# Optimization experiments

Hardware: AMD Instinct MI355X
Metric: run time of the kernel (lower is better)

The kernel has to match this reference:

```python
import jax, jax.numpy as jnp
import numpy as np
from math import sqrt

N_HEADS = 4
IN_FEATURES = 64
KQ = 64
HEAD_V = IN_FEATURES // N_HEADS  # 16


def setup_inputs() -> dict:
    key = jax.random.key(0)
    ks = jax.random.split(key, 7)
    s = 0.05
    x = jax.random.normal(ks[0], (8192, IN_FEATURES), dtype=jnp.float32)
    # Per-head Linear weights stacked on a leading head axis.
    # torch Linear: y = x @ W.T + b; we store W already transposed: [H, F, E]
    Wq = jax.random.normal(ks[1], (N_HEADS, IN_FEATURES, KQ), dtype=jnp.float32) * s
    bq = jax.random.normal(ks[2], (N_HEADS, KQ), dtype=jnp.float32) * s
    Wk = jax.random.normal(ks[3], (N_HEADS, IN_FEATURES, KQ), dtype=jnp.float32) * s
    bk = jax.random.normal(ks[4], (N_HEADS, KQ), dtype=jnp.float32) * s
    Wv = jax.random.normal(ks[5], (N_HEADS, IN_FEATURES, HEAD_V), dtype=jnp.float32) * s
    bv = jax.random.normal(ks[6], (N_HEADS, HEAD_V), dtype=jnp.float32) * s
    return {"x": x, "Wq": Wq, "bq": bq, "Wk": Wk, "bk": bk, "Wv": Wv, "bv": bv}


def reference(x, Wq, bq, Wk, bk, Wv, bv):
    N, F = x.shape
    scale = 1.0 / sqrt(F)  # original divides by sqrt(in_features), NOT sqrt(kq)
    # Batched-head projections: [H, N, E]
    Q = jnp.einsum('nf,hfe->hne', x, Wq) + bq[:, None, :]
    K = jnp.einsum('nf,hfe->hne', x, Wk) + bk[:, None, :]
    V = jnp.einsum('nf,hfd->hnd', x, Wv) + bv[:, None, :]
    logits = jnp.einsum('hne,hme->hnm', Q, K) * scale  # [H, N, N]
    attn = jax.nn.softmax(logits, axis=-1)
    out_heads = jnp.einsum('hnm,hmd->hnd', attn, V)    # [H, N, HEAD_V]
    # Head i writes columns [i*HEAD_V:(i+1)*HEAD_V] of the output.
    out = jnp.transpose(out_heads, (1, 0, 2)).reshape(N, F)
    return out
```

## Files before the change

kernel.cpp:

```cpp
#include <hip/hip_runtime.h>

typedef __attribute__((ext_vector_type(4))) float f32x4;
typedef __attribute__((ext_vector_type(8))) short bf16x8;
typedef __attribute__((ext_vector_type(4))) short bf16x4;
typedef long fp8x8;

#define NH 4

static __device__ __forceinline__ unsigned short f2bf(float f){
  unsigned u = __float_as_uint(f);
  u += 0x7FFFu + ((u >> 16) & 1u);
  return (unsigned short)(u >> 16);
}

static __device__ __forceinline__ unsigned pack2bf(float a, float b){
  return __builtin_amdgcn_perm(__float_as_uint(b) + 0x8000u,
                               __float_as_uint(a) + 0x8000u, 0x07060302u);
}

static __device__ __forceinline__ unsigned pack2bf_t(float a, float b){
  return __builtin_amdgcn_perm(__float_as_uint(b), __float_as_uint(a), 0x07060302u);
}

static __device__ __forceinline__ int pack_fp8x4(float a, float b, float c, float d){
  int w = __builtin_amdgcn_cvt_pk_fp8_f32(a, b, 0, false);
  w     = __builtin_amdgcn_cvt_pk_fp8_f32(c, d, w, true);
  return w;
}

__global__ __launch_bounds__(256) void wprep_kernel(
    const float* __restrict__ Wq, const float* __restrict__ bq,
    const float* __restrict__ Wk, const float* __restrict__ bk,
    const float* __restrict__ Wv,
    unsigned short* __restrict__ WF, float* __restrict__ bias_s, int n)
{
  __shared__ unsigned short wqT[64*72];
  __shared__ unsigned short wkT[64*72];
  __shared__ unsigned short wvT[16*72];

  const int t = threadIdx.x;
  const int h = blockIdx.x;
  const float S1 = 0.4246609001f;
  const int f = t >> 2, eg = t & 3;

  {
    const float4* g = (const float4*)(Wq + h*4096 + f*64 + eg*16);
    #pragma unroll
    for (int p = 0; p < 4; ++p){
      float4 d = g[p];
      int e0 = eg*16 + p*4;
      wqT[(e0+0)*72 + f] = f2bf(d.x * S1);
      wqT[(e0+1)*72 + f] = f2bf(d.y * S1);
      wqT[(e0+2)*72 + f] = f2bf(d.z * S1);
      wqT[(e0+3)*72 + f] = f2bf(d.w * S1);
    }
  }
  {
    const float4* g = (const float4*)(Wk + h*4096 + f*64 + eg*16);
    #pragma unroll
    for (int p = 0; p < 4; ++p){
      float4 d = g[p];
      int e0 = eg*16 + p*4;
      wkT[(e0+0)*72 + f] = f2bf(d.x * S1);
      wkT[(e0+1)*72 + f] = f2bf(d.y * S1);
      wkT[(e0+2)*72 + f] = f2bf(d.z * S1);
      wkT[(e0+3)*72 + f] = f2bf(d.w * S1);
    }
  }
  {
    float4 d = *(const float4*)(Wv + h*1024 + f*16 + eg*4);
    int d0 = eg*4;
    wvT[(d0+0)*72 + f] = f2bf(d.x);
    wvT[(d0+1)*72 + f] = f2bf(d.y);
    wvT[(d0+2)*72 + f] = f2bf(d.z);
    wvT[(d0+3)*72 + f] = f2bf(d.w);
  }
  if (t < 64)       bias_s[h*128 + t] = bq[h*64 + t] * S1;
  else if (t < 128) bias_s[h*128 + t] = bk[h*64 + (t-64)] * S1;
  __syncthreads();

  const int lane = t & 63, w = t >> 6;
  const int quad = lane >> 4, l16 = lane & 15;
  for (int s = w; s < 18; s += 4){
    const unsigned short* src;
    if (s < 8){      int et = s>>1,     ks = s&1;     src = wqT + (et*16+l16)*72 + ks*32 + quad*8; }
    else if (s < 16){int ft = (s-8)>>1, ks = (s-8)&1; src = wkT + (ft*16+l16)*72 + ks*32 + quad*8; }
    else {           int ks = s-16;                   src = wvT + l16*72 + ks*32 + quad*8; }
    uint4 v = *(const uint4*)src;
    *(uint4*)(WF + ((size_t)(h*18 + s)*64 + lane)*8) = v;
  }
}

__global__ __launch_bounds__(256) void proj_kernel(
    const float* __restrict__ x, const float* __restrict__ bv,
    const unsigned short* __restrict__ WF, const float* __restrict__ bias_s,
    unsigned char* __restrict__ Qfr, unsigned char* __restrict__ Kt,
    unsigned short* __restrict__ Vt, int n)
{
  __shared__ unsigned short xf[8*64*8];
  __shared__ float bql[64], bkl[64], bvl[16];

  const int t  = threadIdx.x;
  const int h  = blockIdx.y;
  const int r0 = blockIdx.x * 64;

  {
    const int r = t >> 2, cg4 = t & 3;
    const float4* g = (const float4*)(x + (size_t)(r0 + r)*64 + cg4*16);
    float4 a = g[0], b = g[1], c = g[2], d = g[3];
    unsigned u0 = pack2bf(a.x,a.y), u1 = pack2bf(a.z,a.w);
    unsigned u2 = pack2bf(b.x,b.y), u3 = pack2bf(b.z,b.w);
    unsigned u4 = pack2bf(c.x,c.y), u5 = pack2bf(c.z,c.w);
    unsigned u6 = pack2bf(d.x,d.y), u7 = pack2bf(d.z,d.w);
    const int it = r >> 4, l16r = r & 15, ks = cg4 >> 1, q0 = (cg4 & 1)*2;
    uint4* dst0 = (uint4*)(xf + ((it*2+ks)*64 + q0*16     + l16r)*8);
    uint4* dst1 = (uint4*)(xf + ((it*2+ks)*64 + (q0+1)*16 + l16r)*8);
    *dst0 = make_uint4(u0,u1,u2,u3);
    *dst1 = make_uint4(u4,u5,u6,u7);
  }
  if (t < 64)        bql[t]     = bias_s[h*128 + t];
  else if (t < 128)  bkl[t-64]  = bias_s[h*128 + t];
  else if (t < 144)  bvl[t-128] = bv[h*16 + (t-128)];
  __syncthreads();

  const int lane = t & 63, w = t >> 6;
  const int quad = lane >> 4, l16 = lane & 15;

  bf16x8 xa[8];
  #pragma unroll
  for (int i = 0; i < 8; ++i)
    xa[i] = *(const bf16x8*)(xf + (i*64 + lane)*8);

  const unsigned short* WFh = WF + (size_t)h*18*64*8;
  bf16x8 wq0 = *(const bf16x8*)(WFh + ((size_t)(     w*2 + 0)*64 + lane)*8);
  bf16x8 wq1 = *(const bf16x8*)(WFh + ((size_t)(     w*2 + 1)*64 + lane)*8);
  bf16x8 wk0 = *(const bf16x8*)(WFh + ((size_t)(8  + w*2 + 0)*64 + lane)*8);
  bf16x8 wk1 = *(const bf16x8*)(WFh + ((size_t)(8  + w*2 + 1)*64 + lane)*8);
  bf16x8 wv0 = *(const bf16x8*)(WFh + ((size_t)16*64 + lane)*8);
  bf16x8 wv1 = *(const bf16x8*)(WFh + ((size_t)17*64 + lane)*8);

  const f32x4 z = {0.f,0.f,0.f,0.f};
  f32x4 accQ[4] = {z,z,z,z};
  f32x4 accK[4] = {z,z,z,z};
  f32x4 accV = z;

  #pragma unroll
  for (int it = 0; it < 4; ++it){
    accQ[it] = __builtin_amdgcn_mfma_f32_16x16x32_bf16(wq0, xa[it*2+0], accQ[it], 0,0,0);
    accQ[it] = __builtin_amdgcn_mfma_f32_16x16x32_bf16(wq1, xa[it*2+1], accQ[it], 0,0,0);
  }
  #pragma unroll
  for (int tt = 0; tt < 4; ++tt){
    accK[tt] = __builtin_amdgcn_mfma_f32_16x16x32_bf16(wk0, xa[tt*2+0], accK[tt], 0,0,0);
    accK[tt] = __builtin_amdgcn_mfma_f32_16x16x32_bf16(wk1, xa[tt*2+1], accK[tt], 0,0,0);
  }
  accV = __builtin_amdgcn_mfma_f32_16x16x32_bf16(xa[w*2+0], wv0, accV, 0,0,0);
  accV = __builtin_amdgcn_mfma_f32_16x16x32_bf16(xa[w*2+1], wv1, accV, 0,0,0);

  {
    const int e0 = w*16 + quad*4;
    const float b0 = bql[e0], b1 = bql[e0+1], b2 = bql[e0+2], b3 = bql[e0+3];
    const int qk = (e0 & 31) >> 3, hf = e0 >> 5, boff = (quad & 1) * 4;
    #pragma unroll
    for (int it = 0; it < 4; ++it){
      unsigned o = pack_fp8x4(accQ[it][0]+b0, accQ[it][1]+b1,
                              accQ[it][2]+b2, accQ[it][3]+b3);
      const int T = (r0 >> 4) + it;
      *(unsigned*)(Qfr + (size_t)h*((size_t)n<<6) + (size_t)T*1024
                       + (qk*16 + l16)*16 + hf*8 + boff) = o;
    }
  }
  {
    const int f0 = w*16 + quad*4;
    const float bk0 = bkl[f0], bk1 = bkl[f0+1], bk2 = bkl[f0+2], bk3 = bkl[f0+3];
    const int qk = (f0 & 31) >> 3, hf = f0 >> 5, boff = (quad & 1) * 4;
    #pragma unroll
    for (int tt = 0; tt < 4; ++tt){
      unsigned o = pack_fp8x4(accK[tt][0]+bk0, accK[tt][1]+bk1,
                              accK[tt][2]+bk2, accK[tt][3]+bk3);
      const int T = (r0 >> 4) + tt;
      *(unsigned*)(Kt + (size_t)h*((size_t)n<<6) + (size_t)T*1024
                      + (qk*16 + l16)*16 + hf*8 + boff) = o;
    }
  }
  {
    float bvv = bvl[l16];
    unsigned v01 = pack2bf(accV[0]+bvv, accV[1]+bvv);
    unsigned v23 = pack2bf(accV[2]+bvv, accV[3]+bvv);
    const int T = (r0 >> 4) + w;
    *(uint2*)(Vt + (size_t)h*((size_t)n<<4)
                 + ((size_t)(T>>1)*64 + lane)*8 + (T&1)*4) = make_uint2(v01, v23);
  }
}

__global__ __launch_bounds__(512, 4) void attn_kernel(
    const unsigned char* __restrict__ Qfr, const unsigned char* __restrict__ Kt,
    const unsigned short* __restrict__ Vt, float* __restrict__ out, int n)
{
  __shared__ float part[7][64][33];

  const int tid  = threadIdx.x;
  const int lane = tid & 63;
  const int jq   = tid >> 6;

  #pragma unroll 1
  for (int i = 0; i < jq; ++i) __builtin_amdgcn_s_sleep(3);

  const int bid  = blockIdx.x;
  const int h    = bid & 3;
  const int iblk = bid >> 2;
  const int l16  = lane & 15, quad = lane >> 4;
  const int i0   = iblk*64;
  const int ntq  = (n >> 3) >> 4;
  const int nch  = ntq >> 1;
  const int tile0 = jq * ntq;

  const unsigned char* qfh = Qfr + (size_t)h*((size_t)n<<6);
  longlong2 q0 = *(const longlong2*)(qfh + (size_t)((i0>>4)    )*1024 + lane*16);
  longlong2 q1 = *(const longlong2*)(qfh + (size_t)((i0>>4) + 1)*1024 + lane*16);
  longlong2 q2 = *(const longlong2*)(qfh + (size_t)((i0>>4) + 2)*1024 + lane*16);
  longlong2 q3 = *(const longlong2*)(qfh + (size_t)((i0>>4) + 3)*1024 + lane*16);
  const fp8x8 qf00 = (fp8x8)q0.x, qf01 = (fp8x8)q0.y;
  const fp8x8 qf10 = (fp8x8)q1.x, qf11 = (fp8x8)q1.y;
  const fp8x8 qf20 = (fp8x8)q2.x, qf21 = (fp8x8)q2.y;
  const fp8x8 qf30 = (fp8x8)q3.x, qf31 = (fp8x8)q3.y;

  const longlong2* ktl = (const longlong2*)(Kt + (size_t)h*((size_t)n<<6)) + (size_t)tile0*64 + lane;
  const uint4*     vtu = (const uint4*)(Vt + (size_t)h*((size_t)n<<4)) + (size_t)(tile0>>1)*64 + lane;

  const f32x4 z = {0.f,0.f,0.f,0.f};
  f32x4 o0 = z, o1 = z, o2 = z, o3 = z;
  f32x4 la0 = z, la1 = z, la2 = z, la3 = z;
  const bf16x8 vones = {(short)0x3F80, (short)0x3F80, (short)0x3F80, (short)0x3F80,
                        (short)0x3F80, (short)0x3F80, (short)0x3F80, (short)0x3F80};

  longlong2 ka0 = ktl[0],   ka1 = ktl[64];
  uint4     va  = vtu[0];
  longlong2 kb0 = ktl[128], kb1 = ktl[192];
  uint4     vb  = vtu[64];

#define ITILE(QA, QB, OO, LL)                                                 \
  {                                                                           \
    f32x4 s = __builtin_amdgcn_mfma_f32_16x16x32_fp8_fp8(a0, QA, z, 0,0,0);   \
    s = __builtin_amdgcn_mfma_f32_16x16x32_fp8_fp8(a1, QB, s, 0,0,0);         \
    f32x4 u = __builtin_amdgcn_mfma_f32_16x16x32_fp8_fp8(b0, QA, z, 0,0,0);   \
    u = __builtin_amdgcn_mfma_f32_16x16x32_fp8_fp8(b1, QB, u, 0,0,0);         \
    float e0 = __builtin_amdgcn_exp2f(s[0]);                                  \
    float e1 = __builtin_amdgcn_exp2f(s[1]);                                  \
    float e2 = __builtin_amdgcn_exp2f(s[2]);                                  \
    float e3 = __builtin_amdgcn_exp2f(s[3]);                                  \
    float f0 = __builtin_amdgcn_exp2f(u[0]);                                  \
    float f1 = __builtin_amdgcn_exp2f(u[1]);                                  \
    float f2 = __builtin_amdgcn_exp2f(u[2]);                                  \
    float f3 = __builtin_amdgcn_exp2f(u[3]);                                  \
    union { uint4 uu; bf16x8 v; } pq;                                         \
    pq.uu = make_uint4(pack2bf_t(e0,e1), pack2bf_t(e2,e3),                    \
                       pack2bf_t(f0,f1), pack2bf_t(f2,f3));                   \
    OO = __builtin_amdgcn_mfma_f32_16x16x32_bf16(pq.v, vfv,   OO, 0,0,0);     \
    LL = __builtin_amdgcn_mfma_f32_16x16x32_bf16(pq.v, vones, LL, 0,0,0);     \
  }

#define ATTN_CHUNK(KA, KB, VV)                                                \
  {                                                                           \
    const fp8x8 a0 = (fp8x8)KA.x, a1 = (fp8x8)KA.y;                           \
    const fp8x8 b0 = (fp8x8)KB.x, b1 = (fp8x8)KB.y;                           \
    union { uint4 uu; bf16x8 v; } vfu; vfu.uu = VV;                           \
    const bf16x8 vfv = vfu.v;                                                 \
    ITILE(qf00, qf01, o0, la0)                                                \
    ITILE(qf10, qf11, o1, la1)                                                \
    ITILE(qf20, qf21, o2, la2)                                                \
    ITILE(qf30, qf31, o3, la3)                                                \
  }

  for (int c = 0; c < nch - 2; c += 2){
    ATTN_CHUNK(ka0, ka1, va)
    ka0 = ktl[256]; ka1 = ktl[320]; va = vtu[128];
    ATTN_CHUNK(kb0, kb1, vb)
    kb0 = ktl[384]; kb1 = ktl[448]; vb = vtu[192];
    ktl += 256; vtu += 128;
    #pragma unroll
    for (int g = 0; g < 12; ++g){
      __builtin_amdgcn_sched_group_barrier(0x008, 2, 0);
      __builtin_amdgcn_sched_group_barrier(0x002, 8, 0);
    }
  }
  ATTN_CHUNK(ka0, ka1, va)
  ATTN_CHUNK(kb0, kb1, vb)
#undef ATTN_CHUNK
#undef ITILE

  if (jq > 0){
    float* p = &part[jq-1][lane][0];
    p[ 0]=o0[0];  p[ 1]=o0[1];  p[ 2]=o0[2];  p[ 3]=o0[3];
    p[ 4]=o1[0];  p[ 5]=o1[1];  p[ 6]=o1[2];  p[ 7]=o1[3];
    p[ 8]=o2[0];  p[ 9]=o2[1];  p[10]=o2[2];  p[11]=o2[3];
    p[12]=o3[0];  p[13]=o3[1];  p[14]=o3[2];  p[15]=o3[3];
    p[16]=la0[0]; p[17]=la0[1]; p[18]=la0[2]; p[19]=la0[3];
    p[20]=la1[0]; p[21]=la1[1]; p[22]=la1[2]; p[23]=la1[3];
    p[24]=la2[0]; p[25]=la2[1]; p[26]=la2[2]; p[27]=la2[3];
    p[28]=la3[0]; p[29]=la3[1]; p[30]=la3[2]; p[31]=la3[3];
  }
  __syncthreads();

  if (jq == 0){
    #pragma unroll
    for (int q = 0; q < 7; ++q){
      const float* r = &part[q][lane][0];
      o0[0] +=r[0];  o0[1] +=r[1];  o0[2] +=r[2];  o0[3] +=r[3];
      o1[0] +=r[4];  o1[1] +=r[5];  o1[2] +=r[6];  o1[3] +=r[7];
      o2[0] +=r[8];  o2[1] +=r[9];  o2[2] +=r[10]; o2[3] +=r[11];
      o3[0] +=r[12]; o3[1] +=r[13]; o3[2] +=r[14]; o3[3] +=r[15];
      la0[0]+=r[16]; la0[1]+=r[17]; la0[2]+=r[18]; la0[3]+=r[19];
      la1[0]+=r[20]; la1[1]+=r[21]; la1[2]+=r[22]; la1[3]+=r[23];
      la2[0]+=r[24]; la2[1]+=r[25]; la2[2]+=r[26]; la2[3]+=r[27];
      la3[0]+=r[28]; la3[1]+=r[29]; la3[2]+=r[30]; la3[3]+=r[31];
    }
    #pragma unroll
    for (int reg = 0; reg < 4; ++reg){
      int i = quad*4 + reg;
      out[(size_t)(i0 +      i)*64 + h*16 + l16] = o0[reg] / la0[reg];
      out[(size_t)(i0 + 16 + i)*64 + h*16 + l16] = o1[reg] / la1[reg];
      out[(size_t)(i0 + 32 + i)*64 + h*16 + l16] = o2[reg] / la2[reg];
      out[(size_t)(i0 + 48 + i)*64 + h*16 + l16] = o3[reg] / la3[reg];
    }
  }
}

extern "C" void kernel_launch(void* const* d_in, const int* in_sizes, int n_in,
                              void* d_out, int out_size, void* d_ws, size_t ws_size,
                              hipStream_t stream) {
  const float* x  = (const float*)d_in[0];
  const float* Wq = (const float*)d_in[1];
  const float* bq = (const float*)d_in[2];
  const float* Wk = (const float*)d_in[3];
  const float* bk = (const float*)d_in[4];
  const float* Wv = (const float*)d_in[5];
  const float* bv = (const float*)d_in[6];
  float* out = (float*)d_out;

  const int n = in_sizes[0] / 64;

  unsigned char* Qfr  = (unsigned char*)d_ws;
  unsigned char* Kt   = Qfr + (size_t)NH*n*64;
  unsigned short* Vt  = (unsigned short*)(Kt + (size_t)NH*n*64);
  unsigned short* WF  = Vt + (size_t)NH*n*16;
  float* bias_s       = (float*)(WF + (size_t)NH*18*64*8);

  wprep_kernel<<<NH, 256, 0, stream>>>(Wq, bq, Wk, bk, Wv, WF, bias_s, n);
  proj_kernel<<<dim3(n/64, NH), 256, 0, stream>>>(x, bv, WF, bias_s, Qfr, Kt, Vt, n);
  attn_kernel<<<dim3((n/64)*NH), 512, 0, stream>>>(Qfr, Kt, Vt, out, n);
}
```

Before: 118.5 us.

## Switch attention to 32x32 MFMA tiles with fused row-sum column

Rewrites the attention inner loop to use 32x32x64 scaled FP8 MFMAs for QK^T and 32x32x16 bf16 MFMAs for PV. Q/K/V are stored in a new 32-row-group layout to match. The softmax denominator now comes from a ones-column placed in the V operand's spare columns, removing the separate row-sum MFMA. permlane32_swap rearranges the probabilities between the two 32-lane halves. The aim is fewer MFMA issues and more work per instruction, at the cost of wasting half the PV tile width and adding select and lane-swap overhead.

```diff
diff --git a/kernel.cpp b/kernel.cpp
--- a/kernel.cpp
+++ b/kernel.cpp
@@ -1,8 +1,10 @@
 #include <hip/hip_runtime.h>
 
 typedef __attribute__((ext_vector_type(4))) float f32x4;
+typedef __attribute__((ext_vector_type(16))) float f32x16;
 typedef __attribute__((ext_vector_type(8))) short bf16x8;
-typedef __attribute__((ext_vector_type(4))) short bf16x4;
+typedef __attribute__((ext_vector_type(8))) int int32x8;
+typedef __attribute__((ext_vector_type(2))) int int32x2;
 typedef long fp8x8;
 
 #define NH 4
@@ -26,6 +28,10 @@
   int w = __builtin_amdgcn_cvt_pk_fp8_f32(a, b, 0, false);
   w     = __builtin_amdgcn_cvt_pk_fp8_f32(c, d, w, true);
   return w;
+}
+
+static __device__ __forceinline__ uint4 selv(bool c, uint4 a, uint4 b){
+  return make_uint4(c?a.x:b.x, c?a.y:b.y, c?a.z:b.z, c?a.w:b.w);
 }
 
 __global__ __launch_bounds__(256) void wprep_kernel(
@@ -47,8 +53,7 @@
     const float4* g = (const float4*)(Wq + h*4096 + f*64 + eg*16);
     #pragma unroll
     for (int p = 0; p < 4; ++p){
-      float4 d = g[p];
-      int e0 = eg*16 + p*4;
+      float4 d = g[p]; int e0 = eg*16 + p*4;
       wqT[(e0+0)*72 + f] = f2bf(d.x * S1);
       wqT[(e0+1)*72 + f] = f2bf(d.y * S1);
       wqT[(e0+2)*72 + f] = f2bf(d.z * S1);
@@ -59,8 +64,7 @@
     const float4* g = (const float4*)(Wk + h*4096 + f*64 + eg*16);
     #pragma unroll
     for (int p = 0; p < 4; ++p){
-      float4 d = g[p];
-      int e0 = eg*16 + p*4;
+      float4 d = g[p]; int e0 = eg*16 + p*4;
       wkT[(e0+0)*72 + f] = f2bf(d.x * S1);
       wkT[(e0+1)*72 + f] = f2bf(d.y * S1);
       wkT[(e0+2)*72 + f] = f2bf(d.z * S1);
@@ -157,39 +161,45 @@
   accV = __builtin_amdgcn_mfma_f32_16x16x32_bf16(xa[w*2+0], wv0, accV, 0,0,0);
   accV = __builtin_amdgcn_mfma_f32_16x16x32_bf16(xa[w*2+1], wv1, accV, 0,0,0);
 
+  const int kh    = w >> 1;
+  const int ebyte = (w & 1)*16 + quad*4;
+
   {
     const int e0 = w*16 + quad*4;
     const float b0 = bql[e0], b1 = bql[e0+1], b2 = bql[e0+2], b3 = bql[e0+3];
-    const int qk = (e0 & 31) >> 3, hf = e0 >> 5, boff = (quad & 1) * 4;
     #pragma unroll
     for (int it = 0; it < 4; ++it){
       unsigned o = pack_fp8x4(accQ[it][0]+b0, accQ[it][1]+b1,
                               accQ[it][2]+b2, accQ[it][3]+b3);
-      const int T = (r0 >> 4) + it;
-      *(unsigned*)(Qfr + (size_t)h*((size_t)n<<6) + (size_t)T*1024
-                       + (qk*16 + l16)*16 + hf*8 + boff) = o;
+      const int qg = (r0 >> 5) + (it >> 1);
+      const int lq = (it & 1)*16 + l16 + 32*kh;
+      *(unsigned*)(Qfr + (size_t)h*((size_t)n<<6)
+                       + ((size_t)(qg*64 + lq))*32 + ebyte) = o;
     }
   }
   {
     const int f0 = w*16 + quad*4;
     const float bk0 = bkl[f0], bk1 = bkl[f0+1], bk2 = bkl[f0+2], bk3 = bkl[f0+3];
-    const int qk = (f0 & 31) >> 3, hf = f0 >> 5, boff = (quad & 1) * 4;
     #pragma unroll
     for (int tt = 0; tt < 4; ++tt){
       unsigned o = pack_fp8x4(accK[tt][0]+bk0, accK[tt][1]+bk1,
                               accK[tt][2]+bk2, accK[tt][3]+bk3);
-      const int T = (r0 >> 4) + tt;
-      *(unsigned*)(Kt + (size_t)h*((size_t)n<<6) + (size_t)T*1024
-                      + (qk*16 + l16)*16 + hf*8 + boff) = o;
-    }
-  }
-  {
+      const int kg = (r0 >> 5) + (tt >> 1);
+      const int lk = (tt & 1)*16 + l16 + 32*kh;
+      *(unsigned*)(Kt + (size_t)h*((size_t)n<<6)
+                      + ((size_t)(kg*64 + lk))*32 + ebyte) = o;
+    }
+  }
+  {
+    const int T = (r0 >> 4) + w;
     float bvv = bvl[l16];
-    unsigned v01 = pack2bf(accV[0]+bvv, accV[1]+bvv);
-    unsigned v23 = pack2bf(accV[2]+bvv, accV[3]+bvv);
-    const int T = (r0 >> 4) + w;
-    *(uint2*)(Vt + (size_t)h*((size_t)n<<4)
-                 + ((size_t)(T>>1)*64 + lane)*8 + (T&1)*4) = make_uint2(v01, v23);
+    #pragma unroll
+    for (int reg = 0; reg < 4; ++reg){
+      const int key = quad*4 + reg;
+      Vt[(size_t)h*((size_t)n<<4)
+         + ((size_t)(T*32 + l16 + 16*(key>>3)))*8 + (key & 7)]
+        = f2bf(accV[reg] + bvv);
+    }
   }
 }
 
@@ -209,96 +219,100 @@
   const int bid  = blockIdx.x;
   const int h    = bid & 3;
   const int iblk = bid >> 2;
-  const int l16  = lane & 15, quad = lane >> 4;
   const int i0   = iblk*64;
-  const int ntq  = (n >> 3) >> 4;
-  const int nch  = ntq >> 1;
-  const int tile0 = jq * ntq;
-
-  const unsigned char* qfh = Qfr + (size_t)h*((size_t)n<<6);
-  longlong2 q0 = *(const longlong2*)(qfh + (size_t)((i0>>4)    )*1024 + lane*16);
-  longlong2 q1 = *(const longlong2*)(qfh + (size_t)((i0>>4) + 1)*1024 + lane*16);
-  longlong2 q2 = *(const longlong2*)(qfh + (size_t)((i0>>4) + 2)*1024 + lane*16);
-  longlong2 q3 = *(const longlong2*)(qfh + (size_t)((i0>>4) + 3)*1024 + lane*16);
-  const fp8x8 qf00 = (fp8x8)q0.x, qf01 = (fp8x8)q0.y;
-  const fp8x8 qf10 = (fp8x8)q1.x, qf11 = (fp8x8)q1.y;
-  const fp8x8 qf20 = (fp8x8)q2.x, qf21 = (fp8x8)q2.y;
-  const fp8x8 qf30 = (fp8x8)q3.x, qf31 = (fp8x8)q3.y;
-
-  const longlong2* ktl = (const longlong2*)(Kt + (size_t)h*((size_t)n<<6)) + (size_t)tile0*64 + lane;
-  const uint4*     vtu = (const uint4*)(Vt + (size_t)h*((size_t)n<<4)) + (size_t)(tile0>>1)*64 + lane;
-
-  const f32x4 z = {0.f,0.f,0.f,0.f};
-  f32x4 o0 = z, o1 = z, o2 = z, o3 = z;
-  f32x4 la0 = z, la1 = z, la2 = z, la3 = z;
-  const bf16x8 vones = {(short)0x3F80, (short)0x3F80, (short)0x3F80, (short)0x3F80,
-                        (short)0x3F80, (short)0x3F80, (short)0x3F80, (short)0x3F80};
-
-  longlong2 ka0 = ktl[0],   ka1 = ktl[64];
-  uint4     va  = vtu[0];
-  longlong2 kb0 = ktl[128], kb1 = ktl[192];
-  uint4     vb  = vtu[64];
-
-#define ITILE(QA, QB, OO, LL)                                                 \
+  const int c31  = lane & 31, hl = lane >> 5;
+  const int nch  = n >> 8;
+
+  const int32x8* qp = (const int32x8*)(Qfr + (size_t)h*((size_t)n<<6));
+  const int qg0 = i0 >> 5;
+  const int32x8 qA = qp[(size_t)qg0*64 + lane];
+  const int32x8 qB = qp[(size_t)(qg0+1)*64 + lane];
+
+  const int32x8* kp = (const int32x8*)(Kt + (size_t)h*((size_t)n<<6))
+                      + (size_t)(jq*32)*64 + lane;
+  const int vlane = (lane & 15) + ((lane & 32) >> 1);
+  const uint4* vp = (const uint4*)(Vt + (size_t)h*((size_t)n<<4))
+                    + (size_t)(jq*64)*32 + vlane;
+
+  const bool  vload = (c31 < 16);
+  const unsigned one2 = 0x3F803F80u;
+  const uint4 vsel = (c31 == 16) ? make_uint4(one2,one2,one2,one2)
+                                 : make_uint4(0,0,0,0);
+
+  const f32x16 z16 = {0,0,0,0,0,0,0,0,0,0,0,0,0,0,0,0};
+  f32x16 acc0 = z16, acc1 = z16;
+
+  int32x8 ka = kp[0], kb = kp[64];
+
+#define PVSTEP(S, ACC, VF0, VF1)                                              \
   {                                                                           \
-    f32x4 s = __builtin_amdgcn_mfma_f32_16x16x32_fp8_fp8(a0, QA, z, 0,0,0);   \
-    s = __builtin_amdgcn_mfma_f32_16x16x32_fp8_fp8(a1, QB, s, 0,0,0);         \
-    f32x4 u = __builtin_amdgcn_mfma_f32_16x16x32_fp8_fp8(b0, QA, z, 0,0,0);   \
-    u = __builtin_amdgcn_mfma_f32_16x16x32_fp8_fp8(b1, QB, u, 0,0,0);         \
-    float e0 = __builtin_amdgcn_exp2f(s[0]);                                  \
-    float e1 = __builtin_amdgcn_exp2f(s[1]);                                  \
-    float e2 = __builtin_amdgcn_exp2f(s[2]);                                  \
-    float e3 = __builtin_amdgcn_exp2f(s[3]);                                  \
-    float f0 = __builtin_amdgcn_exp2f(u[0]);                                  \
-    float f1 = __builtin_amdgcn_exp2f(u[1]);                                  \
-    float f2 = __builtin_amdgcn_exp2f(u[2]);                                  \
-    float f3 = __builtin_amdgcn_exp2f(u[3]);                                  \
-    union { uint4 uu; bf16x8 v; } pq;                                         \
-    pq.uu = make_uint4(pack2bf_t(e0,e1), pack2bf_t(e2,e3),                    \
-                       pack2bf_t(f0,f1), pack2bf_t(f2,f3));                   \
-    OO = __builtin_amdgcn_mfma_f32_16x16x32_bf16(pq.v, vfv,   OO, 0,0,0);     \
-    LL = __builtin_amdgcn_mfma_f32_16x16x32_bf16(pq.v, vones, LL, 0,0,0);     \
-  }
-
-#define ATTN_CHUNK(KA, KB, VV)                                                \
+    float p0  = __builtin_amdgcn_exp2f(S[0]);                                 \
+    float p1  = __builtin_amdgcn_exp2f(S[1]);                                 \
+    float p2  = __builtin_amdgcn_exp2f(S[2]);                                 \
+    float p3  = __builtin_amdgcn_exp2f(S[3]);                                 \
+    float p4  = __builtin_amdgcn_exp2f(S[4]);                                 \
+    float p5  = __builtin_amdgcn_exp2f(S[5]);                                 \
+    float p6  = __builtin_amdgcn_exp2f(S[6]);                                 \
+    float p7  = __builtin_amdgcn_exp2f(S[7]);                                 \
+    float p8  = __builtin_amdgcn_exp2f(S[8]);                                 \
+    float p9  = __builtin_amdgcn_exp2f(S[9]);                                 \
+    float p10 = __builtin_amdgcn_exp2f(S[10]);                                \
+    float p11 = __builtin_amdgcn_exp2f(S[11]);                                \
+    float p12 = __builtin_amdgcn_exp2f(S[12]);                                \
+    float p13 = __builtin_amdgcn_exp2f(S[13]);                                \
+    float p14 = __builtin_amdgcn_exp2f(S[14]);                                \
+    float p15 = __builtin_amdgcn_exp2f(S[15]);                                \
+    unsigned u0 = pack2bf_t(p0,p1),   u1 = pack2bf_t(p2,p3);                  \
+    unsigned u2 = pack2bf_t(p4,p5),   u3 = pack2bf_t(p6,p7);                  \
+    unsigned u4 = pack2bf_t(p8,p9),   u5 = pack2bf_t(p10,p11);                \
+    unsigned u6 = pack2bf_t(p12,p13), u7 = pack2bf_t(p14,p15);                \
+    int32x2 r01 = __builtin_amdgcn_permlane32_swap((int)u0,(int)u2,false,false);\
+    int32x2 r23 = __builtin_amdgcn_permlane32_swap((int)u1,(int)u3,false,false);\
+    int32x2 r45 = __builtin_amdgcn_permlane32_swap((int)u4,(int)u6,false,false);\
+    int32x2 r67 = __builtin_amdgcn_permlane32_swap((int)u5,(int)u7,false,false);\
+    union { uint4 uu; bf16x8 v; } pa1, pa2;                                   \
+    pa1.uu = make_uint4(r01[0], r23[0], r01[1], r23[1]);                      \
+    pa2.uu = make_uint4(r45[0], r67[0], r45[1], r67[1]);                      \
+    ACC = __builtin_amdgcn_mfma_f32_32x32x16_bf16(pa1.v, VF0, ACC, 0,0,0);    \
+    ACC = __builtin_amdgcn_mfma_f32_32x32x16_bf16(pa2.v, VF1, ACC, 0,0,0);    \
+  }
+
+#define CHUNKV(KF, VIDX)                                                      \
   {                                                                           \
-    const fp8x8 a0 = (fp8x8)KA.x, a1 = (fp8x8)KA.y;                           \
-    const fp8x8 b0 = (fp8x8)KB.x, b1 = (fp8x8)KB.y;                           \
-    union { uint4 uu; bf16x8 v; } vfu; vfu.uu = VV;                           \
-    const bf16x8 vfv = vfu.v;                                                 \
-    ITILE(qf00, qf01, o0, la0)                                                \
-    ITILE(qf10, qf11, o1, la1)                                                \
-    ITILE(qf20, qf21, o2, la2)                                                \
-    ITILE(qf30, qf31, o3, la3)                                                \
+    union { uint4 uu; bf16x8 v; } v0u, v1u;                                   \
+    v0u.uu = selv(vload, vp[(VIDX)],      vsel);                              \
+    v1u.uu = selv(vload, vp[(VIDX) + 32], vsel);                              \
+    f32x16 s0 = __builtin_amdgcn_mfma_scale_f32_32x32x64_f8f6f4(              \
+        KF, qA, z16, 0, 0, 0, 0x7F7F7F7F, 0, 0x7F7F7F7F);                     \
+    f32x16 s1 = __builtin_amdgcn_mfma_scale_f32_32x32x64_f8f6f4(              \
+        KF, qB, z16, 0, 0, 0, 0x7F7F7F7F, 0, 0x7F7F7F7F);                     \
+    PVSTEP(s0, acc0, v0u.v, v1u.v)                                            \
+    PVSTEP(s1, acc1, v0u.v, v1u.v)                                            \
   }
 
   for (int c = 0; c < nch - 2; c += 2){
-    ATTN_CHUNK(ka0, ka1, va)
-    ka0 = ktl[256]; ka1 = ktl[320]; va = vtu[128];
-    ATTN_CHUNK(kb0, kb1, vb)
-    kb0 = ktl[384]; kb1 = ktl[448]; vb = vtu[192];
-    ktl += 256; vtu += 128;
+    CHUNKV(ka, 0)
+    ka = kp[128];
+    CHUNKV(kb, 64)
+    kb = kp[192];
+    kp += 128; vp += 128;
     #pragma unroll
     for (int g = 0; g < 12; ++g){
-      __builtin_amdgcn_sched_group_barrier(0x008, 2, 0);
-      __builtin_amdgcn_sched_group_barrier(0x002, 8, 0);
-    }
-  }
-  ATTN_CHUNK(ka0, ka1, va)
-  ATTN_CHUNK(kb0, kb1, vb)
-#undef ATTN_CHUNK
-#undef ITILE
+      __builtin_amdgcn_sched_group_barrier(0x008, 1, 0);
+      __builtin_amdgcn_sched_group_barrier(0x002, 10, 0);
+    }
+  }
+  CHUNKV(ka, 0)
+  CHUNKV(kb, 64)
+#undef CHUNKV
+#undef PVSTEP
 
   if (jq > 0){
     float* p = &part[jq-1][lane][0];
-    p[ 0]=o0[0];  p[ 1]=o0[1];  p[ 2]=o0[2];  p[ 3]=o0[3];
-    p[ 4]=o1[0];  p[ 5]=o1[1];  p[ 6]=o1[2];  p[ 7]=o1[3];
-    p[ 8]=o2[0];  p[ 9]=o2[1];  p[10]=o2[2];  p[11]=o2[3];
-    p[12]=o3[0];  p[13]=o3[1];  p[14]=o3[2];  p[15]=o3[3];
-    p[16]=la0[0]; p[17]=la0[1]; p[18]=la0[2]; p[19]=la0[3];
-    p[20]=la1[0]; p[21]=la1[1]; p[22]=la1[2]; p[23]=la1[3];
-    p[24]=la2[0]; p[25]=la2[1]; p[26]=la2[2]; p[27]=la2[3];
-    p[28]=la3[0]; p[29]=la3[1]; p[30]=la3[2]; p[31]=la3[3];
+    #pragma unroll
+    for (int i = 0; i < 16; ++i) p[i]      = acc0[i];
+    #pragma unroll
+    for (int i = 0; i < 16; ++i) p[16 + i] = acc1[i];
   }
   __syncthreads();
 
@@ -306,22 +320,21 @@
     #pragma unroll
     for (int q = 0; q < 7; ++q){
       const float* r = &part[q][lane][0];
-      o0[0] +=r[0];  o0[1] +=r[1];  o0[2] +=r[2];  o0[3] +=r[3];
-      o1[0] +=r[4];  o1[1] +=r[5];  o1[2] +=r[6];  o1[3] +=r[7];
-      o2[0] +=r[8];  o2[1] +=r[9];  o2[2] +=r[10]; o2[3] +=r[11];
-      o3[0] +=r[12]; o3[1] +=r[13]; o3[2] +=r[14]; o3[3] +=r[15];
-      la0[0]+=r[16]; la0[1]+=r[17]; la0[2]+=r[18]; la0[3]+=r[19];
-      la1[0]+=r[20]; la1[1]+=r[21]; la1[2]+=r[22]; la1[3]+=r[23];
-      la2[0]+=r[24]; la2[1]+=r[25]; la2[2]+=r[26]; la2[3]+=r[27];
-      la3[0]+=r[28]; la3[1]+=r[29]; la3[2]+=r[30]; la3[3]+=r[31];
-    }
-    #pragma unroll
-    for (int reg = 0; reg < 4; ++reg){
-      int i = quad*4 + reg;
-      out[(size_t)(i0 +      i)*64 + h*16 + l16] = o0[reg] / la0[reg];
-      out[(size_t)(i0 + 16 + i)*64 + h*16 + l16] = o1[reg] / la1[reg];
-      out[(size_t)(i0 + 32 + i)*64 + h*16 + l16] = o2[reg] / la2[reg];
-      out[(size_t)(i0 + 48 + i)*64 + h*16 + l16] = o3[reg] / la3[reg];
+      #pragma unroll
+      for (int i = 0; i < 16; ++i) acc0[i] += r[i];
+      #pragma unroll
+      for (int i = 0; i < 16; ++i) acc1[i] += r[16 + i];
+    }
+    const int lsrc = 16 | (lane & 32);
+    #pragma unroll
+    for (int i = 0; i < 16; ++i){
+      float la0 = __shfl(acc0[i], lsrc, 64);
+      float la1 = __shfl(acc1[i], lsrc, 64);
+      const int row = (i & 3) + 8*(i >> 2) + 4*hl;
+      if (c31 < 16){
+        out[(size_t)(i0 +      row)*64 + h*16 + c31] = acc0[i] / la0;
+        out[(size_t)(i0 + 32 + row)*64 + h*16 + c31] = acc1[i] / la1;
+      }
     }
   }
 }
```

Result: slower. 151.7 us (+28.0%).
